# Performance work log

Hardware: AMD Instinct MI355X
Metric: run time of the kernel (lower is better)

## Reference

```python
import jax, jax.numpy as jnp
import numpy as np

N_HEADS = 32
N_KV_HEADS = 8
THETA = 10000.0


def _rope_tables(head_dim, seq_len):
    # freqs: [head_dim//2]
    freqs = 1.0 / (THETA ** (jnp.arange(0, head_dim, 2, dtype=jnp.float32) / head_dim))
    ang = jnp.arange(seq_len, dtype=jnp.float32)[:, None] * freqs[None, :]  # [T, hd/2]
    return jnp.cos(ang), jnp.sin(ang)


def _apply_rope(x, cos, sin):
    # x: [B, T, H, hd]; cos/sin: [T, hd/2] -> broadcast [1, T, 1, hd/2]
    x_even = x[..., 0::2]
    x_odd = x[..., 1::2]
    c = cos[None, :, None, :]
    s = sin[None, :, None, :]
    out_even = x_even * c - x_odd * s
    out_odd = x_even * s + x_odd * c
    # interleave back to [..., hd]
    out = jnp.stack([out_even, out_odd], axis=-1)
    return out.reshape(x.shape)


def setup_inputs() -> dict:
    key = jax.random.key(0)
    ks = jax.random.split(key, 5)
    B, T, C = 2, 2048, 2048
    kv_dim = (C // N_HEADS) * N_KV_HEADS  # 512
    sc = 1.0 / np.sqrt(C)
    return {
        "x": jax.random.normal(ks[0], (B, T, C), dtype=jnp.float32),
        "wq": jax.random.normal(ks[1], (C, C), dtype=jnp.float32) * sc,
        "wk": jax.random.normal(ks[2], (C, kv_dim), dtype=jnp.float32) * sc,
        "wv": jax.random.normal(ks[3], (C, kv_dim), dtype=jnp.float32) * sc,
        "wo": jax.random.normal(ks[4], (C, C), dtype=jnp.float32) * sc,
    }


def reference(x, wq, wk, wv, wo):
    B, T, C = x.shape
    hd = C // N_HEADS
    rep = N_HEADS // N_KV_HEADS

    q = (x @ wq).reshape(B, T, N_HEADS, hd)
    k = (x @ wk).reshape(B, T, N_KV_HEADS, hd)
    v = (x @ wv).reshape(B, T, N_KV_HEADS, hd)

    cos, sin = _rope_tables(hd, T)
    q = _apply_rope(q, cos, sin)
    k = _apply_rope(k, cos, sin)

    q = q.transpose(0, 2, 1, 3)  # [B, H, T, hd]
    k = k.transpose(0, 2, 1, 3)  # [B, KV, T, hd]
    v = v.transpose(0, 2, 1, 3)

    # GQA: repeat_interleave kv heads to match q heads
    k = jnp.repeat(k, rep, axis=1)
    v = jnp.repeat(v, rep, axis=1)

    scores = jnp.einsum("bhtd,bhsd->bhts", q, k) / jnp.sqrt(jnp.float32(hd))
    weights = jax.nn.softmax(scores, axis=-1)  # no causal mask, as in source
    out = jnp.einsum("bhts,bhsd->bhtd", weights, v)
    out = out.transpose(0, 2, 1, 3).reshape(B, T, C)
    return out @ wo
```

## Files before the change

kernel.cpp:

```cpp
#include <hip/hip_runtime.h>
#include <hip/hip_bf16.h>


typedef unsigned short u16;
typedef short bf16x8 __attribute__((ext_vector_type(8)));
typedef float f32x4 __attribute__((ext_vector_type(4)));

#define LOG2E 1.4426950408889634f
#define NFREQ (-13.287712379549449f / 32.f)

#if __has_builtin(__builtin_amdgcn_exp2f)
#define EXP2F(x) __builtin_amdgcn_exp2f(x)
#else
#define EXP2F(x) exp2f(x)
#endif

__device__ __forceinline__ float bf2f(u16 u) {
    union { unsigned v; float f; } x; x.v = ((unsigned)u) << 16; return x.f;
}
__device__ __forceinline__ u16 f2bf(float f) {
    unsigned u = __float_as_uint(f);
    u += 0x7fffu + ((u >> 16) & 1u);
    return (u16)(u >> 16);
}
__device__ __forceinline__ u16 f2bf_fast(float f) {
    return (u16)((__float_as_uint(f) + 0x8000u) >> 16);
}

__device__ __forceinline__ void async_copy16(const void* g, void* l) {
    __builtin_amdgcn_global_load_lds((const __attribute__((address_space(1))) void*)g,
                                     (__attribute__((address_space(3))) void*)l, 16, 0, 0);
}

__global__ void cast_bf16_kernel(const float* __restrict__ in, u16* __restrict__ out, size_t n4) {
    for (size_t i = blockIdx.x * (size_t)blockDim.x + threadIdx.x; i < n4;
         i += (size_t)gridDim.x * blockDim.x) {
        float4 v = ((const float4*)in)[i];
        ushort4 o;
        o.x = f2bf(v.x); o.y = f2bf(v.y); o.z = f2bf(v.z); o.w = f2bf(v.w);
        ((ushort4*)out)[i] = o;
    }
}

__global__ void rope_table_kernel(float2* __restrict__ tab) {
    int idx = blockIdx.x * blockDim.x + threadIdx.x;
    int t = idx >> 5, i = idx & 31;
    float freq = exp2f((float)i * NFREQ);
    float s, c;
    sincosf((float)t * freq, &s, &c);
    tab[idx] = make_float2(c, s);
}

__global__ void transpose_cast4_kernel(const float* __restrict__ wq, const float* __restrict__ wk,
                                       const float* __restrict__ wv, const float* __restrict__ wo,
                                       u16* __restrict__ wqkvT, u16* __restrict__ woT) {
    const int K = 2048;
    const float* W; u16* Wt; int N;
    switch (blockIdx.z) {
        case 0:  W = wq; Wt = wqkvT;                        N = 2048; break;
        case 1:  W = wk; Wt = wqkvT + (size_t)2048 * 2048;  N = 512;  break;
        case 2:  W = wv; Wt = wqkvT + (size_t)2560 * 2048;  N = 512;  break;
        default: W = wo; Wt = woT;                          N = 2048; break;
    }
    if ((int)blockIdx.x * 32 >= N) return;
    __shared__ float tile[32][33];
    int x = blockIdx.x * 32 + threadIdx.x;
    int y0 = blockIdx.y * 32 + threadIdx.y;
    #pragma unroll
    for (int r = 0; r < 32; r += 8)
        tile[threadIdx.y + r][threadIdx.x] = W[(size_t)(y0 + r) * N + x];
    __syncthreads();
    int xo = blockIdx.y * 32 + threadIdx.x;
    int yo0 = blockIdx.x * 32 + threadIdx.y;
    #pragma unroll
    for (int r = 0; r < 32; r += 8)
        Wt[(size_t)(yo0 + r) * K + xo] = f2bf(tile[threadIdx.x][threadIdx.y + r]);
}

__global__ void transpose_bf16_kernel(const u16* __restrict__ in, u16* __restrict__ out,
                                      int R, int C) {
    __shared__ u16 tile[32][33];
    int x = blockIdx.x * 32 + threadIdx.x;
    int y0 = blockIdx.y * 32;
    #pragma unroll
    for (int r = threadIdx.y; r < 32; r += 8)
        tile[r][threadIdx.x] = in[(size_t)(y0 + r) * C + x];
    __syncthreads();
    int xo = y0 + threadIdx.x;
    int yo = blockIdx.x * 32;
    #pragma unroll
    for (int r = threadIdx.y; r < 32; r += 8)
        out[(size_t)(yo + r) * R + xo] = tile[threadIdx.x][r];
}

__global__ __launch_bounds__(256) void gemm_qkv_kernel(const u16* __restrict__ A,
                                                       const u16* __restrict__ Bt,
                                                       u16* __restrict__ qout,
                                                       u16* __restrict__ kout,
                                                       u16* __restrict__ vout,
                                                       const float2* __restrict__ rope_tab,
                                                       int K) {
    __shared__ __align__(16) u16 As[128 * 64];
    __shared__ __align__(16) u16 Bs[128 * 64];
    const int tid = threadIdx.x;
    const int m0 = blockIdx.y * 128;
    const int n0 = blockIdx.x * 128;
    const int w = tid >> 6, lane = tid & 63;
    const int quad = lane >> 4, ln = lane & 15;
    const int wr = (w >> 1) * 64, wc = (w & 1) * 64;

    f32x4 acc[4][4];
    #pragma unroll
    for (int i = 0; i < 4; i++)
        #pragma unroll
        for (int j = 0; j < 4; j++) acc[i][j] = (f32x4){0.f, 0.f, 0.f, 0.f};

    for (int kt = 0; kt < K; kt += 64) {
        #pragma unroll
        for (int p = 0; p < 4; p++) {
            int chunk = p * 256 + tid;
            int r = chunk >> 3, cl = chunk & 7;
            int cg = cl ^ (r & 7);
            async_copy16(&A[(size_t)(m0 + r) * K + kt + cg * 8], &As[chunk * 8]);
            async_copy16(&Bt[(size_t)(n0 + r) * K + kt + cg * 8], &Bs[chunk * 8]);
        }
        __syncthreads();
        #pragma unroll
        for (int kk = 0; kk < 2; kk++) {
            bf16x8 a[4], b[4];
            #pragma unroll
            for (int i = 0; i < 4; i++) {
                int r = wr + i * 16 + ln;
                int cl = (kk * 4 + quad) ^ (ln & 7);
                a[i] = *(const bf16x8*)(&As[r * 64 + cl * 8]);
            }
            #pragma unroll
            for (int j = 0; j < 4; j++) {
                int r = wc + j * 16 + ln;
                int cl = (kk * 4 + quad) ^ (ln & 7);
                b[j] = *(const bf16x8*)(&Bs[r * 64 + cl * 8]);
            }
            #pragma unroll
            for (int i = 0; i < 4; i++)
                #pragma unroll
                for (int j = 0; j < 4; j++)
                    acc[i][j] = __builtin_amdgcn_mfma_f32_16x16x32_bf16(a[i], b[j], acc[i][j], 0, 0, 0);
        }
        __syncthreads();
    }

    int nb = n0 + wc;
    u16* dst; int ldc, coff; bool isv = false; float scale = 1.f;
    if (nb < 2048)      { dst = qout; ldc = 2048; coff = 0;    scale = 0.125f * LOG2E; }
    else if (nb < 2560) { dst = kout; ldc = 512;  coff = 2048; }
    else                { dst = vout; ldc = 512;  coff = 2560; isv = true; }

    if (isv) {
        #pragma unroll
        for (int i = 0; i < 4; i++)
            #pragma unroll
            for (int r = 0; r < 4; r++) {
                int row = m0 + wr + i * 16 + quad * 4 + r;
                #pragma unroll
                for (int j = 0; j < 4; j++)
                    dst[(size_t)row * ldc + nb + j * 16 + ln - coff] = f2bf(acc[i][j][r]);
            }
    } else {
        float fsin = (ln & 1) ? 1.f : -1.f;
        int fidx[4];
        #pragma unroll
        for (int j = 0; j < 4; j++)
            fidx[j] = ((nb + j * 16 + ln) & 63) >> 1;
        #pragma unroll
        for (int i = 0; i < 4; i++)
            #pragma unroll
            for (int r = 0; r < 4; r++) {
                int row = m0 + wr + i * 16 + quad * 4 + r;
                const float2* trow = rope_tab + (size_t)(row & 2047) * 32;
                #pragma unroll
                for (int j = 0; j < 4; j++) {
                    float v = acc[i][j][r];
                    float p = __shfl_xor(v, 1, 64);
                    float2 cs = trow[fidx[j]];
                    float rr = (v * cs.x + fsin * p * cs.y) * scale;
                    dst[(size_t)row * ldc + nb + j * 16 + ln - coff] = f2bf(rr);
                }
            }
    }
}

__global__ __launch_bounds__(256) void gemm_bt_kernel(const u16* __restrict__ A,
                                                      const u16* __restrict__ Bt,
                                                      float* __restrict__ C,
                                                      int M, int N, int K) {
    __shared__ __align__(16) u16 As[128 * 64];
    __shared__ __align__(16) u16 Bs[128 * 64];
    const int tid = threadIdx.x;
    const int m0 = blockIdx.y * 128;
    const int n0 = blockIdx.x * 128;
    const int w = tid >> 6, lane = tid & 63;
    const int quad = lane >> 4, ln = lane & 15;
    const int wr = (w >> 1) * 64, wc = (w & 1) * 64;

    f32x4 acc[4][4];
    #pragma unroll
    for (int i = 0; i < 4; i++)
        #pragma unroll
        for (int j = 0; j < 4; j++) acc[i][j] = (f32x4){0.f, 0.f, 0.f, 0.f};

    for (int kt = 0; kt < K; kt += 64) {
        #pragma unroll
        for (int p = 0; p < 4; p++) {
            int chunk = p * 256 + tid;
            int r = chunk >> 3, cl = chunk & 7;
            int cg = cl ^ (r & 7);
            async_copy16(&A[(size_t)(m0 + r) * K + kt + cg * 8], &As[chunk * 8]);
            async_copy16(&Bt[(size_t)(n0 + r) * K + kt + cg * 8], &Bs[chunk * 8]);
        }
        __syncthreads();
        #pragma unroll
        for (int kk = 0; kk < 2; kk++) {
            bf16x8 a[4], b[4];
            #pragma unroll
            for (int i = 0; i < 4; i++) {
                int r = wr + i * 16 + ln;
                int cl = (kk * 4 + quad) ^ (ln & 7);
                a[i] = *(const bf16x8*)(&As[r * 64 + cl * 8]);
            }
            #pragma unroll
            for (int j = 0; j < 4; j++) {
                int r = wc + j * 16 + ln;
                int cl = (kk * 4 + quad) ^ (ln & 7);
                b[j] = *(const bf16x8*)(&Bs[r * 64 + cl * 8]);
            }
            #pragma unroll
            for (int i = 0; i < 4; i++)
                #pragma unroll
                for (int j = 0; j < 4; j++)
                    acc[i][j] = __builtin_amdgcn_mfma_f32_16x16x32_bf16(a[i], b[j], acc[i][j], 0, 0, 0);
        }
        __syncthreads();
    }
    #pragma unroll
    for (int i = 0; i < 4; i++)
        #pragma unroll
        for (int r = 0; r < 4; r++) {
            int row = m0 + wr + i * 16 + quad * 4 + r;
            #pragma unroll
            for (int j = 0; j < 4; j++)
                C[(size_t)row * N + n0 + wc + j * 16 + ln] = acc[i][j][r];
        }
}

__global__ __launch_bounds__(256) void attn_kernel(const u16* __restrict__ qb,
                                                   const u16* __restrict__ kb,
                                                   const u16* __restrict__ vtb,
                                                   u16* __restrict__ ob) {
    const int T = 2048;
    const int CQ = 2048, CKV = 512;
    __shared__ __align__(16) u16 smem[4096 + 4096 + 4 * 32 * 40];
    u16* Ks = smem;
    u16* Vt = smem + 4096;
    u16* Ps = smem + 8192;

    const int tid = threadIdx.x;
    const int bh = blockIdx.y;
    const int b = bh >> 5, h = bh & 31, kvh = h >> 2;
    const int t0 = blockIdx.x * 128;
    const u16* qbase = qb + ((size_t)(b * T + t0) * CQ + h * 64);
    const u16* kbase = kb + ((size_t)(b * T) * CKV + kvh * 64);
    const u16* vtbase = vtb + ((size_t)(kvh * 64)) * 4096 + b * 2048;

    const int w = tid >> 6, lane = tid & 63, quad = lane >> 4, ln = lane & 15;
    u16* Pw = &Ps[w * 32 * 40];

    bf16x8 ones;
    #pragma unroll
    for (int e = 0; e < 8; e++) ones[e] = (short)0x3F80;

    #pragma unroll
    for (int p = 0; p < 4; p++) {
        int chunk = p * 256 + tid;
        int r = chunk >> 3, cl = chunk & 7;
        int cg = cl ^ (r & 7);
        async_copy16(&qbase[(size_t)r * CQ + cg * 8], &smem[chunk * 8]);
    }
    __syncthreads();
    bf16x8 qf[2][2];
    #pragma unroll
    for (int i = 0; i < 2; i++)
        #pragma unroll
        for (int kk = 0; kk < 2; kk++) {
            int r = w * 32 + i * 16 + ln;
            int cl = (kk * 4 + quad) ^ (ln & 7);
            qf[i][kk] = *(const bf16x8*)(&smem[r * 64 + cl * 8]);
        }
    __syncthreads();

    f32x4 o_acc[2][4];
    f32x4 l_acc[2];
    #pragma unroll
    for (int i = 0; i < 2; i++) {
        l_acc[i] = (f32x4){0.f, 0.f, 0.f, 0.f};
        #pragma unroll
        for (int j = 0; j < 4; j++) o_acc[i][j] = (f32x4){0.f, 0.f, 0.f, 0.f};
    }

    for (int st = 0; st < T; st += 64) {
        #pragma unroll
        for (int p = 0; p < 2; p++) {
            int chunk = p * 256 + tid;
            int r = chunk >> 3, cl = chunk & 7;
            int cg = cl ^ (r & 7);
            async_copy16(&kbase[(size_t)(st + r) * CKV + cg * 8], &Ks[chunk * 8]);
            async_copy16(&vtbase[(size_t)r * 4096 + st + cg * 8], &Vt[chunk * 8]);
        }
        __syncthreads();

        f32x4 s_acc[2][4];
        #pragma unroll
        for (int i = 0; i < 2; i++)
            #pragma unroll
            for (int j = 0; j < 4; j++) s_acc[i][j] = (f32x4){0.f, 0.f, 0.f, 0.f};
        #pragma unroll
        for (int kk = 0; kk < 2; kk++) {
            bf16x8 bfr[4];
            #pragma unroll
            for (int j = 0; j < 4; j++) {
                int r = j * 16 + ln;
                int cl = (kk * 4 + quad) ^ (ln & 7);
                bfr[j] = *(const bf16x8*)(&Ks[r * 64 + cl * 8]);
            }
            #pragma unroll
            for (int i = 0; i < 2; i++)
                #pragma unroll
                for (int j = 0; j < 4; j++)
                    s_acc[i][j] = __builtin_amdgcn_mfma_f32_16x16x32_bf16(qf[i][kk], bfr[j], s_acc[i][j], 0, 0, 0);
        }

        #pragma unroll
        for (int h2 = 0; h2 < 2; h2++) {
            #pragma unroll
            for (int i = 0; i < 2; i++)
                #pragma unroll
                for (int rr = 0; rr < 4; rr++) {
                    int row = i * 16 + quad * 4 + rr;
                    #pragma unroll
                    for (int jj = 0; jj < 2; jj++) {
                        float pv = EXP2F(s_acc[i][h2 * 2 + jj][rr]);
                        Pw[row * 40 + jj * 16 + ln] = f2bf_fast(pv);
                    }
                }
            bf16x8 pa[2], vb[4];
            #pragma unroll
            for (int i = 0; i < 2; i++)
                pa[i] = *(const bf16x8*)(&Pw[(i * 16 + ln) * 40 + quad * 8]);
            #pragma unroll
            for (int jd = 0; jd < 4; jd++) {
                int d = jd * 16 + ln;
                int cl = (h2 * 4 + quad) ^ (d & 7);
                vb[jd] = *(const bf16x8*)(&Vt[d * 64 + cl * 8]);
            }
            #pragma unroll
            for (int i = 0; i < 2; i++) {
                l_acc[i] = __builtin_amdgcn_mfma_f32_16x16x32_bf16(pa[i], ones, l_acc[i], 0, 0, 0);
                #pragma unroll
                for (int jd = 0; jd < 4; jd++)
                    o_acc[i][jd] = __builtin_amdgcn_mfma_f32_16x16x32_bf16(pa[i], vb[jd], o_acc[i][jd], 0, 0, 0);
            }
        }
        __syncthreads();
    }

    #pragma unroll
    for (int i = 0; i < 2; i++)
        #pragma unroll
        for (int rr = 0; rr < 4; rr++) {
            float linv = 1.f / l_acc[i][rr];
            int row = w * 32 + i * 16 + quad * 4 + rr;
            #pragma unroll
            for (int jd = 0; jd < 4; jd++) {
                int col = jd * 16 + ln;
                ob[(size_t)(b * T + t0 + row) * CQ + h * 64 + col] = f2bf(o_acc[i][jd][rr] * linv);
            }
        }
}

#define WS_X_BF   ((size_t)0)
#define WS_WQKVT  ((size_t)16777216)
#define WS_WOT    ((size_t)29360128)
#define WS_QBF    ((size_t)37748736)
#define WS_KBF    ((size_t)54525952)
#define WS_VBF    ((size_t)58720256)
#define WS_ABF    ((size_t)62914560)

extern "C" void kernel_launch(void* const* d_in, const int* in_sizes, int n_in,
                              void* d_out, int out_size, void* d_ws, size_t ws_size,
                              hipStream_t stream) {
    const float* x  = (const float*)d_in[0];
    const float* wq = (const float*)d_in[1];
    const float* wk = (const float*)d_in[2];
    const float* wv = (const float*)d_in[3];
    const float* wo = (const float*)d_in[4];
    char* ws = (char*)d_ws;
    u16* xbf   = (u16*)(ws + WS_X_BF);
    u16* wqkvT = (u16*)(ws + WS_WQKVT);
    u16* woT   = (u16*)(ws + WS_WOT);
    u16* qbf   = (u16*)(ws + WS_QBF);
    u16* kbf   = (u16*)(ws + WS_KBF);
    u16* vbf   = (u16*)(ws + WS_VBF);
    u16* vtbf  = (u16*)(ws + WS_X_BF);
    u16* abf   = (u16*)(ws + WS_ABF);
    float2* rtab = (float2*)(ws + WS_ABF);
    float* out = (float*)d_out;

    cast_bf16_kernel<<<2048, 256, 0, stream>>>(x, xbf, (size_t)4096 * 2048 / 4);
    rope_table_kernel<<<256, 256, 0, stream>>>(rtab);
    transpose_cast4_kernel<<<dim3(64, 64, 4), dim3(32, 8), 0, stream>>>(wq, wk, wv, wo, wqkvT, woT);

    gemm_qkv_kernel<<<dim3(24, 32), 256, 0, stream>>>(xbf, wqkvT, qbf, kbf, vbf, rtab, 2048);

    transpose_bf16_kernel<<<dim3(16, 128), dim3(32, 8), 0, stream>>>(vbf, vtbf, 4096, 512);

    attn_kernel<<<dim3(16, 64), 256, 0, stream>>>(qbf, kbf, vtbf, abf);

    gemm_bt_kernel<<<dim3(16, 32), 256, 0, stream>>>(abf, woT, out, 4096, 2048, 2048);
}
```

Measured before the change: 356.0 us.

## Merge prep kernels, enlarge attention key tile, permute V layout, pack P stores

```diff
diff --git a/kernel.cpp b/kernel.cpp
--- a/kernel.cpp
+++ b/kernel.cpp
@@ -23,8 +23,10 @@
     u += 0x7fffu + ((u >> 16) & 1u);
     return (u16)(u >> 16);
 }
-__device__ __forceinline__ u16 f2bf_fast(float f) {
-    return (u16)((__float_as_uint(f) + 0x8000u) >> 16);
+__device__ __forceinline__ unsigned pack_bf16x2(float lo, float hi) {
+    unsigned ul = (__float_as_uint(lo) + 0x8000u) >> 16;
+    unsigned uh = (__float_as_uint(hi) + 0x8000u) & 0xffff0000u;
+    return uh | ul;
 }
 
 __device__ __forceinline__ void async_copy16(const void* g, void* l) {
@@ -32,65 +34,73 @@
                                      (__attribute__((address_space(3))) void*)l, 16, 0, 0);
 }
 
-__global__ void cast_bf16_kernel(const float* __restrict__ in, u16* __restrict__ out, size_t n4) {
-    for (size_t i = blockIdx.x * (size_t)blockDim.x + threadIdx.x; i < n4;
-         i += (size_t)gridDim.x * blockDim.x) {
-        float4 v = ((const float4*)in)[i];
-        ushort4 o;
-        o.x = f2bf(v.x); o.y = f2bf(v.y); o.z = f2bf(v.z); o.w = f2bf(v.w);
-        ((ushort4*)out)[i] = o;
-    }
-}
-
-__global__ void rope_table_kernel(float2* __restrict__ tab) {
-    int idx = blockIdx.x * blockDim.x + threadIdx.x;
-    int t = idx >> 5, i = idx & 31;
-    float freq = exp2f((float)i * NFREQ);
-    float s, c;
-    sincosf((float)t * freq, &s, &c);
-    tab[idx] = make_float2(c, s);
-}
-
-__global__ void transpose_cast4_kernel(const float* __restrict__ wq, const float* __restrict__ wk,
-                                       const float* __restrict__ wv, const float* __restrict__ wo,
-                                       u16* __restrict__ wqkvT, u16* __restrict__ woT) {
-    const int K = 2048;
-    const float* W; u16* Wt; int N;
-    switch (blockIdx.z) {
-        case 0:  W = wq; Wt = wqkvT;                        N = 2048; break;
-        case 1:  W = wk; Wt = wqkvT + (size_t)2048 * 2048;  N = 512;  break;
-        case 2:  W = wv; Wt = wqkvT + (size_t)2560 * 2048;  N = 512;  break;
-        default: W = wo; Wt = woT;                          N = 2048; break;
-    }
-    if ((int)blockIdx.x * 32 >= N) return;
-    __shared__ float tile[32][33];
-    int x = blockIdx.x * 32 + threadIdx.x;
-    int y0 = blockIdx.y * 32 + threadIdx.y;
-    #pragma unroll
-    for (int r = 0; r < 32; r += 8)
-        tile[threadIdx.y + r][threadIdx.x] = W[(size_t)(y0 + r) * N + x];
-    __syncthreads();
-    int xo = blockIdx.y * 32 + threadIdx.x;
-    int yo0 = blockIdx.x * 32 + threadIdx.y;
-    #pragma unroll
-    for (int r = 0; r < 32; r += 8)
-        Wt[(size_t)(yo0 + r) * K + xo] = f2bf(tile[threadIdx.x][threadIdx.y + r]);
-}
-
-__global__ void transpose_bf16_kernel(const u16* __restrict__ in, u16* __restrict__ out,
+__global__ void prep_kernel(const float* __restrict__ x,
+                            const float* __restrict__ wq, const float* __restrict__ wk,
+                            const float* __restrict__ wv, const float* __restrict__ wo,
+                            u16* __restrict__ xbf, u16* __restrict__ wqkvT,
+                            u16* __restrict__ woT, float2* __restrict__ rtab) {
+    const int bz = blockIdx.z;
+    if (bz < 4) {
+        const int K = 2048;
+        const float* W; u16* Wt; int N;
+        switch (bz) {
+            case 0:  W = wq; Wt = wqkvT;                        N = 2048; break;
+            case 1:  W = wk; Wt = wqkvT + (size_t)2048 * 2048;  N = 512;  break;
+            case 2:  W = wv; Wt = wqkvT + (size_t)2560 * 2048;  N = 512;  break;
+            default: W = wo; Wt = woT;                          N = 2048; break;
+        }
+        if ((int)blockIdx.x * 32 >= N) return;
+        __shared__ float tile[32][33];
+        int xx = blockIdx.x * 32 + threadIdx.x;
+        int y0 = blockIdx.y * 32 + threadIdx.y;
+        #pragma unroll
+        for (int r = 0; r < 32; r += 8)
+            tile[threadIdx.y + r][threadIdx.x] = W[(size_t)(y0 + r) * N + xx];
+        __syncthreads();
+        int xo = blockIdx.y * 32 + threadIdx.x;
+        int yo0 = blockIdx.x * 32 + threadIdx.y;
+        #pragma unroll
+        for (int r = 0; r < 32; r += 8)
+            Wt[(size_t)(yo0 + r) * K + xo] = f2bf(tile[threadIdx.x][threadIdx.y + r]);
+    } else if (bz == 4) {
+        int bid = blockIdx.y * gridDim.x + blockIdx.x;
+        int tid = threadIdx.y * 32 + threadIdx.x;
+        const size_t n4 = (size_t)4096 * 2048 / 4;
+        for (size_t i = (size_t)bid * 256 + tid; i < n4; i += (size_t)4096 * 256) {
+            float4 v = ((const float4*)x)[i];
+            ushort4 o;
+            o.x = f2bf(v.x); o.y = f2bf(v.y); o.z = f2bf(v.z); o.w = f2bf(v.w);
+            ((ushort4*)xbf)[i] = o;
+        }
+    } else {
+        int bid = blockIdx.y * gridDim.x + blockIdx.x;
+        int idx = bid * 256 + threadIdx.y * 32 + threadIdx.x;
+        if (idx < 2048 * 32) {
+            int t = idx >> 5, i = idx & 31;
+            float freq = exp2f((float)i * NFREQ);
+            float s, c;
+            sincosf((float)t * freq, &s, &c);
+            rtab[idx] = make_float2(c, s);
+        }
+    }
+}
+
+__global__ void transpose_perm_kernel(const u16* __restrict__ in, u16* __restrict__ out,
                                       int R, int C) {
     __shared__ u16 tile[32][33];
-    int x = blockIdx.x * 32 + threadIdx.x;
+    int xx = blockIdx.x * 32 + threadIdx.x;
     int y0 = blockIdx.y * 32;
     #pragma unroll
     for (int r = threadIdx.y; r < 32; r += 8)
-        tile[r][threadIdx.x] = in[(size_t)(y0 + r) * C + x];
+        tile[r][threadIdx.x] = in[(size_t)(y0 + r) * C + xx];
     __syncthreads();
-    int xo = y0 + threadIdx.x;
+    int s = y0 + threadIdx.x;
+    int c = s & 63;
+    int sp = (s & ~63) | (c & 32) | ((c & 15) << 1) | ((c >> 4) & 1);
     int yo = blockIdx.x * 32;
     #pragma unroll
     for (int r = threadIdx.y; r < 32; r += 8)
-        out[(size_t)(yo + r) * R + xo] = tile[threadIdx.x][r];
+        out[(size_t)(yo + r) * R + sp] = tile[threadIdx.x][r];
 }
 
 __global__ __launch_bounds__(256) void gemm_qkv_kernel(const u16* __restrict__ A,
@@ -258,10 +268,9 @@
                                                    u16* __restrict__ ob) {
     const int T = 2048;
     const int CQ = 2048, CKV = 512;
-    __shared__ __align__(16) u16 smem[4096 + 4096 + 4 * 32 * 40];
-    u16* Ks = smem;
-    u16* Vt = smem + 4096;
-    u16* Ps = smem + 8192;
+    __shared__ __align__(16) u16 Ks[128 * 64];
+    __shared__ __align__(16) u16 Vt[64 * 128];
+    __shared__ __align__(16) u16 Ps[4 * 32 * 72];
 
     const int tid = threadIdx.x;
     const int bh = blockIdx.y;
@@ -272,30 +281,18 @@
     const u16* vtbase = vtb + ((size_t)(kvh * 64)) * 4096 + b * 2048;
 
     const int w = tid >> 6, lane = tid & 63, quad = lane >> 4, ln = lane & 15;
-    u16* Pw = &Ps[w * 32 * 40];
+    u16* Pw = &Ps[w * 32 * 72];
 
     bf16x8 ones;
     #pragma unroll
     for (int e = 0; e < 8; e++) ones[e] = (short)0x3F80;
 
-    #pragma unroll
-    for (int p = 0; p < 4; p++) {
-        int chunk = p * 256 + tid;
-        int r = chunk >> 3, cl = chunk & 7;
-        int cg = cl ^ (r & 7);
-        async_copy16(&qbase[(size_t)r * CQ + cg * 8], &smem[chunk * 8]);
-    }
-    __syncthreads();
     bf16x8 qf[2][2];
     #pragma unroll
     for (int i = 0; i < 2; i++)
         #pragma unroll
-        for (int kk = 0; kk < 2; kk++) {
-            int r = w * 32 + i * 16 + ln;
-            int cl = (kk * 4 + quad) ^ (ln & 7);
-            qf[i][kk] = *(const bf16x8*)(&smem[r * 64 + cl * 8]);
-        }
-    __syncthreads();
+        for (int kk = 0; kk < 2; kk++)
+            qf[i][kk] = *(const bf16x8*)(&qbase[(size_t)(w * 32 + i * 16 + ln) * CQ + kk * 32 + quad * 8]);
 
     f32x4 o_acc[2][4];
     f32x4 l_acc[2];
@@ -306,27 +303,29 @@
         for (int j = 0; j < 4; j++) o_acc[i][j] = (f32x4){0.f, 0.f, 0.f, 0.f};
     }
 
-    for (int st = 0; st < T; st += 64) {
-        #pragma unroll
-        for (int p = 0; p < 2; p++) {
+    for (int st = 0; st < T; st += 128) {
+        #pragma unroll
+        for (int p = 0; p < 4; p++) {
             int chunk = p * 256 + tid;
             int r = chunk >> 3, cl = chunk & 7;
             int cg = cl ^ (r & 7);
             async_copy16(&kbase[(size_t)(st + r) * CKV + cg * 8], &Ks[chunk * 8]);
-            async_copy16(&vtbase[(size_t)r * 4096 + st + cg * 8], &Vt[chunk * 8]);
-        }
-        __syncthreads();
-
-        f32x4 s_acc[2][4];
+            int d = chunk >> 4, cl2 = chunk & 15;
+            int cg2 = cl2 ^ (d & 7);
+            async_copy16(&vtbase[(size_t)d * 4096 + st + cg2 * 8], &Vt[chunk * 8]);
+        }
+        __syncthreads();
+
+        f32x4 s_acc[2][8];
         #pragma unroll
         for (int i = 0; i < 2; i++)
             #pragma unroll
-            for (int j = 0; j < 4; j++) s_acc[i][j] = (f32x4){0.f, 0.f, 0.f, 0.f};
+            for (int j = 0; j < 8; j++) s_acc[i][j] = (f32x4){0.f, 0.f, 0.f, 0.f};
         #pragma unroll
         for (int kk = 0; kk < 2; kk++) {
-            bf16x8 bfr[4];
-            #pragma unroll
-            for (int j = 0; j < 4; j++) {
+            bf16x8 bfr[8];
+            #pragma unroll
+            for (int j = 0; j < 8; j++) {
                 int r = j * 16 + ln;
                 int cl = (kk * 4 + quad) ^ (ln & 7);
                 bfr[j] = *(const bf16x8*)(&Ks[r * 64 + cl * 8]);
@@ -334,7 +333,7 @@
             #pragma unroll
             for (int i = 0; i < 2; i++)
                 #pragma unroll
-                for (int j = 0; j < 4; j++)
+                for (int j = 0; j < 8; j++)
                     s_acc[i][j] = __builtin_amdgcn_mfma_f32_16x16x32_bf16(qf[i][kk], bfr[j], s_acc[i][j], 0, 0, 0);
         }
 
@@ -345,28 +344,34 @@
                 #pragma unroll
                 for (int rr = 0; rr < 4; rr++) {
                     int row = i * 16 + quad * 4 + rr;
+                    unsigned* prow = (unsigned*)&Pw[row * 72];
+                    float v0 = EXP2F(s_acc[i][h2 * 4 + 0][rr]);
+                    float v1 = EXP2F(s_acc[i][h2 * 4 + 1][rr]);
+                    float v2 = EXP2F(s_acc[i][h2 * 4 + 2][rr]);
+                    float v3 = EXP2F(s_acc[i][h2 * 4 + 3][rr]);
+                    prow[ln]      = pack_bf16x2(v0, v1);
+                    prow[16 + ln] = pack_bf16x2(v2, v3);
+                }
+            #pragma unroll
+            for (int kk = 0; kk < 2; kk++) {
+                bf16x8 pa[2], vb[4];
+                #pragma unroll
+                for (int i = 0; i < 2; i++)
+                    pa[i] = *(const bf16x8*)(&Pw[(i * 16 + ln) * 72 + kk * 32 + quad * 8]);
+                #pragma unroll
+                for (int jd = 0; jd < 4; jd++) {
+                    int d = jd * 16 + ln;
+                    int cg = h2 * 8 + kk * 4 + quad;
+                    int cl = (cg & 8) | ((cg ^ (d & 7)) & 7);
+                    vb[jd] = *(const bf16x8*)(&Vt[d * 128 + cl * 8]);
+                }
+                #pragma unroll
+                for (int i = 0; i < 2; i++) {
+                    l_acc[i] = __builtin_amdgcn_mfma_f32_16x16x32_bf16(pa[i], ones, l_acc[i], 0, 0, 0);
                     #pragma unroll
-                    for (int jj = 0; jj < 2; jj++) {
-                        float pv = EXP2F(s_acc[i][h2 * 2 + jj][rr]);
-                        Pw[row * 40 + jj * 16 + ln] = f2bf_fast(pv);
-                    }
+                    for (int jd = 0; jd < 4; jd++)
+                        o_acc[i][jd] = __builtin_amdgcn_mfma_f32_16x16x32_bf16(pa[i], vb[jd], o_acc[i][jd], 0, 0, 0);
                 }
-            bf16x8 pa[2], vb[4];
-            #pragma unroll
-            for (int i = 0; i < 2; i++)
-                pa[i] = *(const bf16x8*)(&Pw[(i * 16 + ln) * 40 + quad * 8]);
-            #pragma unroll
-            for (int jd = 0; jd < 4; jd++) {
-                int d = jd * 16 + ln;
-                int cl = (h2 * 4 + quad) ^ (d & 7);
-                vb[jd] = *(const bf16x8*)(&Vt[d * 64 + cl * 8]);
-            }
-            #pragma unroll
-            for (int i = 0; i < 2; i++) {
-                l_acc[i] = __builtin_amdgcn_mfma_f32_16x16x32_bf16(pa[i], ones, l_acc[i], 0, 0, 0);
-                #pragma unroll
-                for (int jd = 0; jd < 4; jd++)
-                    o_acc[i][jd] = __builtin_amdgcn_mfma_f32_16x16x32_bf16(pa[i], vb[jd], o_acc[i][jd], 0, 0, 0);
             }
         }
         __syncthreads();
@@ -414,13 +419,12 @@
     float2* rtab = (float2*)(ws + WS_ABF);
     float* out = (float*)d_out;
 
-    cast_bf16_kernel<<<2048, 256, 0, stream>>>(x, xbf, (size_t)4096 * 2048 / 4);
-    rope_table_kernel<<<256, 256, 0, stream>>>(rtab);
-    transpose_cast4_kernel<<<dim3(64, 64, 4), dim3(32, 8), 0, stream>>>(wq, wk, wv, wo, wqkvT, woT);
+    prep_kernel<<<dim3(64, 64, 6), dim3(32, 8), 0, stream>>>(x, wq, wk, wv, wo,
+                                                             xbf, wqkvT, woT, rtab);
 
     gemm_qkv_kernel<<<dim3(24, 32), 256, 0, stream>>>(xbf, wqkvT, qbf, kbf, vbf, rtab, 2048);
 
-    transpose_bf16_kernel<<<dim3(16, 128), dim3(32, 8), 0, stream>>>(vbf, vtbf, 4096, 512);
+    transpose_perm_kernel<<<dim3(16, 128), dim3(32, 8), 0, stream>>>(vbf, vtbf, 4096, 512);
 
     attn_kernel<<<dim3(16, 64), 256, 0, stream>>>(qbf, kbf, vtbf, abf);
 
```

Result: faster. 338.5 us (-4.9%).
